# Performance work log

Measured on AMD Instinct MI355X. Metric: run time of the kernel, lower is better.

## Reference

```python
import jax, jax.numpy as jnp
import numpy as np

B, D, F, H = 256, 9, 8, 256   # batch of trees, tree depth, input features, hidden
N = 2 ** (D + 1) - 1          # total nodes per full binary tree (heap layout)


def _init(key, shape, fan_in):
    return jax.random.normal(key, shape, jnp.float32) * (1.0 / np.sqrt(fan_in))


def setup_inputs() -> dict:
    key = jax.random.key(0)
    ks = jax.random.split(key, 6)
    return {
        "data": jax.random.normal(ks[0], (B, N, F), jnp.float32),
        "Wu": _init(ks[1], (H, F), F),
        "bu": jnp.zeros((H,), jnp.float32),
        "Wr": _init(ks[2], (3 * H, 3 * H), 3 * H),
        "br": jnp.zeros((3 * H,), jnp.float32),
        "Wh": _init(ks[3], (H, 3 * H), 3 * H),
        "bh": jnp.zeros((H,), jnp.float32),
        "Wz": _init(ks[4], (4 * H, 4 * H), 4 * H),
        "bz": jnp.zeros((4 * H,), jnp.float32),
        "Wp": _init(ks[5], (1, H), H),
        "bp": jnp.zeros((1,), jnp.float32),
    }


def reference(data, Wu, bu, Wr, br, Wh, bh, Wz, bz, Wp, bp):
    # data: [B, N, F] node features in heap (level-order) layout;
    # children of the i-th node of level l are nodes 2i, 2i+1 of level l+1.
    b, n_nodes, _ = data.shape
    L = (n_nodes + 1) // 2          # number of leaves
    depth = L.bit_length() - 1
    h_dim = Wu.shape[0]

    # leaf embedding u for every node (leaf() is applied at every tree node)
    u = jnp.einsum('bnf,hf->bnh', data, Wu) + bu          # [B, N, H]
    h = u[:, L - 1:, :]                                    # leaf level states [B, L, H]

    for l in range(depth - 1, -1, -1):                     # bottom-up over levels
        n = 2 ** l
        parent = u[:, n - 1:2 * n - 1, :]                  # [B, n, H]
        h_l, h_r = h[:, 0::2, :], h[:, 1::2, :]            # [B, n, H] each
        hhu = jnp.concatenate([parent, h_l, h_r], axis=-1)  # [B, n, 3H]
        r = jax.nn.sigmoid(jnp.einsum('bnk,jk->bnj', hhu, Wr) + br)
        h_new = jax.nn.relu(jnp.einsum('bnk,hk->bnh', r * hhu, Wh) + bh)
        hhhu = jnp.concatenate([h_new, hhu], axis=-1)      # [B, n, 4H]
        zlin = jnp.einsum('bnk,jk->bnj', hhhu, Wz) + bz    # [B, n, 4H]
        z = jax.nn.softmax(zlin.reshape(b, n, 4, h_dim), axis=2)
        h = (z * hhhu.reshape(b, n, 4, h_dim)).sum(axis=2)  # gated combine -> [B, n, H]

    # h is [B, 1, H] at the root; logits head
    logits = jnp.einsum('bnh,oh->bno', h, Wp) + bp          # [B, 1, 1]
    return logits[:, 0, 0]                                  # [B]
```

## Files before the change

kernel.cpp:

```cpp
#include <hip/hip_runtime.h>
#include <math.h>

#define BB 256
#define NN 1023
#define FF 8
#define HH 256
#define DEPTH 9

enum { EPI_NONE = 0, EPI_SIGMUL = 1, EPI_RELU = 2, EPI_COMBINE = 3 };

typedef __bf16 bf16x8_t __attribute__((ext_vector_type(8)));
typedef float f32x4_t __attribute__((ext_vector_type(4)));

__device__ __forceinline__ void stage16(const void* g, void* l) {
    __builtin_amdgcn_global_load_lds(
        (const __attribute__((address_space(1))) void*)g,
        (__attribute__((address_space(3))) void*)l,
        16, 0, 0);
}

__device__ __forceinline__ int xcd_remap(int hw, int nwg) {
    const int xcd = hw & 7, k0 = hw >> 3;
    const int qq = nwg >> 3, rr = nwg & 7;
    return (xcd < rr ? xcd * (qq + 1) : rr * (qq + 1) + (xcd - rr) * qq) + k0;
}

template <int EPI>
__global__ __launch_bounds__(1024, 4) void gemm256w(
    const __bf16* __restrict__ A, int lda,
    const __bf16* __restrict__ W,
    const float* __restrict__ bias,
    const __bf16* __restrict__ aux, int ldaux,
    void* __restrict__ Cout, int ldc,
    int K)
{
    __shared__ __bf16 lds[2][2][256 * 64];
    const int tid = threadIdx.x;
    const int lane = tid & 63;
    const int w = tid >> 6;
    const int wr = w >> 2, wc = w & 3;

    const int nwg = gridDim.x * gridDim.y;
    const int hw = blockIdx.y * gridDim.x + blockIdx.x;
    const int wg = xcd_remap(hw, nwg);
    const int bm0 = (wg / gridDim.x) * 256;
    const int bn0 = (wg % gridDim.x) * 256;

    const int srow = tid >> 3;
    const int scolz = ((tid & 7) ^ (srow & 7)) * 8;

    f32x4_t acc[4][4];
#pragma unroll
    for (int i = 0; i < 4; ++i)
#pragma unroll
        for (int j = 0; j < 4; ++j) acc[i][j] = (f32x4_t){0.f, 0.f, 0.f, 0.f};

    const int rA = lane & 15;
    const int klane = (lane >> 4) * 8;
    const int rxor = (lane & 7) * 8;
    const int NT = K >> 6;

#define STAGE_T(t, buf)                                                        \
    do {                                                                       \
        const int kk_ = (t) << 6;                                              \
        stage16(A + (size_t)(bm0 + srow) * lda + kk_ + scolz,                  \
                &lds[buf][0][w * 512]);                                        \
        stage16(A + (size_t)(bm0 + 128 + srow) * lda + kk_ + scolz,            \
                &lds[buf][0][8192 + w * 512]);                                 \
        stage16(W + (size_t)(bn0 + srow) * K + kk_ + scolz,                    \
                &lds[buf][1][w * 512]);                                        \
        stage16(W + (size_t)(bn0 + 128 + srow) * K + kk_ + scolz,              \
                &lds[buf][1][8192 + w * 512]);                                 \
    } while (0)
#define LDA_F(As_, i, ks) \
    (*(const bf16x8_t*)&(As_)[(wr * 64 + (i) * 16 + rA) * 64 + (((ks) * 32 + klane) ^ rxor)])
#define LDB_F(Bs_, j, ks) \
    (*(const bf16x8_t*)&(Bs_)[(wc * 64 + (j) * 16 + rA) * 64 + (((ks) * 32 + klane) ^ rxor)])

    STAGE_T(0, 0);
    STAGE_T(1, 1);
    asm volatile("s_waitcnt vmcnt(4)" ::: "memory");
    __builtin_amdgcn_s_barrier();

    for (int t = 0; t < NT; ++t) {
        const int cur = t & 1;
        const __bf16* As = lds[cur][0];
        const __bf16* Bs = lds[cur][1];
        bf16x8_t af[4], bf[4];

#pragma unroll
        for (int j = 0; j < 4; ++j) bf[j] = LDB_F(Bs, j, 0);
#pragma unroll
        for (int i = 0; i < 4; ++i) af[i] = LDA_F(As, i, 0);
#pragma unroll
        for (int i = 0; i < 4; ++i)
#pragma unroll
            for (int j = 0; j < 4; ++j)
                acc[i][j] = __builtin_amdgcn_mfma_f32_16x16x32_bf16(
                    af[i], bf[j], acc[i][j], 0, 0, 0);
#pragma unroll
        for (int j = 0; j < 4; ++j) bf[j] = LDB_F(Bs, j, 1);
#pragma unroll
        for (int i = 0; i < 4; ++i) af[i] = LDA_F(As, i, 1);
#pragma unroll
        for (int i = 0; i < 2; ++i)
#pragma unroll
            for (int j = 0; j < 4; ++j)
                acc[i][j] = __builtin_amdgcn_mfma_f32_16x16x32_bf16(
                    af[i], bf[j], acc[i][j], 0, 0, 0);

        asm volatile("s_waitcnt lgkmcnt(0)" ::: "memory");
        __builtin_amdgcn_s_barrier();
        if (t + 2 < NT) STAGE_T(t + 2, cur);

        __builtin_amdgcn_s_setprio(1);
#pragma unroll
        for (int i = 2; i < 4; ++i)
#pragma unroll
            for (int j = 0; j < 4; ++j)
                acc[i][j] = __builtin_amdgcn_mfma_f32_16x16x32_bf16(
                    af[i], bf[j], acc[i][j], 0, 0, 0);
        __builtin_amdgcn_s_setprio(0);

        if (t + 1 < NT) {
            if (t + 2 < NT) {
                asm volatile("s_waitcnt vmcnt(4)" ::: "memory");
            } else {
                asm volatile("s_waitcnt vmcnt(0)" ::: "memory");
            }
            __builtin_amdgcn_s_barrier();
        }
    }
#undef STAGE_T
#undef LDA_F
#undef LDB_F

    const int hi = lane >> 4;
    const int r = lane & 15;

    if (EPI == EPI_COMBINE) {
        __bf16* pan = &lds[0][0][0];
        const int g0 = bn0 >> 2;
        float bz4[4];
#pragma unroll
        for (int g = 0; g < 4; ++g) bz4[g] = bias[bn0 + wc * 64 + g * 16 + r];
        const int G = g0 + wc * 16 + r;
#pragma unroll
        for (int i = 0; i < 4; ++i) {
#pragma unroll
            for (int reg = 0; reg < 4; ++reg) {
                const int lr = wr * 64 + i * 16 + hi * 4 + reg;
                const int gr = bm0 + lr;
                float z0 = acc[i][0][reg] + bz4[0];
                float z1 = acc[i][1][reg] + bz4[1];
                float z2 = acc[i][2][reg] + bz4[2];
                float z3 = acc[i][3][reg] + bz4[3];
                float mx = fmaxf(fmaxf(z0, z1), fmaxf(z2, z3));
                float e0 = __expf(z0 - mx), e1 = __expf(z1 - mx);
                float e2 = __expf(z2 - mx), e3 = __expf(z3 - mx);
                const __bf16* hrow = aux + (size_t)gr * ldaux + G;
                float hv = (e0 * (float)hrow[0] + e1 * (float)hrow[256] +
                            e2 * (float)hrow[512] + e3 * (float)hrow[768]) /
                           (e0 + e1 + e2 + e3);
                pan[lr * 72 + wc * 16 + r] = (__bf16)hv;
            }
        }
        __syncthreads();
#pragma unroll
        for (int it = 0; it < 2; ++it) {
            const int unit = it * 1024 + tid;
            const int row = unit >> 3;
            const int c8 = (unit & 7) * 8;
            bf16x8_t vv = *(const bf16x8_t*)&pan[row * 72 + c8];
            *(bf16x8_t*)((__bf16*)Cout + (size_t)(bm0 + row) * ldc + g0 + c8) = vv;
        }
    } else if (EPI == EPI_SIGMUL) {
        __bf16* pan = &lds[0][0][0];
        float bv[4];
#pragma unroll
        for (int j = 0; j < 4; ++j) bv[j] = bias[bn0 + wc * 64 + j * 16 + r];
#pragma unroll
        for (int j = 0; j < 4; ++j) {
            const int lc = wc * 64 + j * 16 + r;
            const int gc = bn0 + lc;
#pragma unroll
            for (int i = 0; i < 4; ++i) {
#pragma unroll
                for (int reg = 0; reg < 4; ++reg) {
                    const int lr = wr * 64 + i * 16 + hi * 4 + reg;
                    const int gr = bm0 + lr;
                    float v = acc[i][j][reg] + bv[j];
                    float s = 1.0f / (1.0f + __expf(-v));
                    v = s * (float)aux[(size_t)gr * ldaux + gc];
                    pan[lr * 256 + lc] = (__bf16)v;
                }
            }
        }
        __syncthreads();
#pragma unroll
        for (int it = 0; it < 8; ++it) {
            const int unit = it * 1024 + tid;
            const int row = unit >> 5;
            const int c8 = (unit & 31) * 8;
            bf16x8_t vv = *(const bf16x8_t*)&pan[row * 256 + c8];
            *(bf16x8_t*)((__bf16*)Cout + (size_t)(bm0 + row) * ldc + bn0 + c8) = vv;
        }
    } else {
#pragma unroll
        for (int j = 0; j < 4; ++j) {
            const int gc = bn0 + wc * 64 + j * 16 + r;
            const float bv = bias[gc];
#pragma unroll
            for (int i = 0; i < 4; ++i) {
#pragma unroll
                for (int reg = 0; reg < 4; ++reg) {
                    const int gr = bm0 + wr * 64 + i * 16 + hi * 4 + reg;
                    float v = acc[i][j][reg] + bv;
                    if (EPI == EPI_RELU) v = fmaxf(v, 0.0f);
                    if (EPI == EPI_RELU)
                        ((__bf16*)Cout)[(size_t)gr * ldc + gc] = (__bf16)v;
                    else
                        ((float*)Cout)[(size_t)gr * ldc + gc] = v;
                }
            }
        }
    }
}

template <int EPI>
__global__ __launch_bounds__(256) void gemm_mfma(
    const __bf16* __restrict__ A, int lda,
    const __bf16* __restrict__ W,
    const float* __restrict__ bias,
    const __bf16* __restrict__ aux, int ldaux,
    void* __restrict__ Cout, int ldc,
    int K)
{
    __shared__ __bf16 As[128 * 32];
    __shared__ __bf16 Bs[128 * 32];
    const int tid = threadIdx.x;
    const int lane = tid & 63;
    const int w = tid >> 6;
    const int wr = w >> 1, wc = w & 1;

    const int nwg = gridDim.x * gridDim.y;
    const int hw = blockIdx.y * gridDim.x + blockIdx.x;
    const int wg = xcd_remap(hw, nwg);
    const int bm0 = (wg / gridDim.x) * 128;
    const int bn0 = (wg % gridDim.x) * 128;

    const int srow = lane >> 2;
    const int scol = (lane & 3) * 8;

    f32x4_t acc[4][4];
#pragma unroll
    for (int i = 0; i < 4; ++i)
#pragma unroll
        for (int j = 0; j < 4; ++j) acc[i][j] = (f32x4_t){0.f, 0.f, 0.f, 0.f};

    const int rA = lane & 15;
    const int kslot = (lane >> 4) * 8;

    for (int kk = 0; kk < K; kk += 32) {
        stage16(A + (size_t)(bm0 + w * 16 + srow) * lda + kk + scol,
                &As[(w * 16) * 32]);
        stage16(A + (size_t)(bm0 + 64 + w * 16 + srow) * lda + kk + scol,
                &As[(64 + w * 16) * 32]);
        stage16(W + (size_t)(bn0 + w * 16 + srow) * K + kk + scol,
                &Bs[(w * 16) * 32]);
        stage16(W + (size_t)(bn0 + 64 + w * 16 + srow) * K + kk + scol,
                &Bs[(64 + w * 16) * 32]);
        __syncthreads();

        bf16x8_t af[4], bfr[4];
#pragma unroll
        for (int i = 0; i < 4; ++i)
            af[i] = *(const bf16x8_t*)&As[(wr * 64 + i * 16 + rA) * 32 + kslot];
#pragma unroll
        for (int j = 0; j < 4; ++j)
            bfr[j] = *(const bf16x8_t*)&Bs[(wc * 64 + j * 16 + rA) * 32 + kslot];
#pragma unroll
        for (int i = 0; i < 4; ++i)
#pragma unroll
            for (int j = 0; j < 4; ++j)
                acc[i][j] = __builtin_amdgcn_mfma_f32_16x16x32_bf16(
                    af[i], bfr[j], acc[i][j], 0, 0, 0);
        __syncthreads();
    }

    if (EPI == EPI_COMBINE) {
        const int r = lane & 15;
        const int G = ((bn0 + wc * 64) >> 2) + r;
        float bz4[4];
#pragma unroll
        for (int g = 0; g < 4; ++g) bz4[g] = bias[bn0 + wc * 64 + g * 16 + r];
#pragma unroll
        for (int i = 0; i < 4; ++i) {
#pragma unroll
            for (int reg = 0; reg < 4; ++reg) {
                const int gr = bm0 + wr * 64 + i * 16 + (lane >> 4) * 4 + reg;
                float z0 = acc[i][0][reg] + bz4[0];
                float z1 = acc[i][1][reg] + bz4[1];
                float z2 = acc[i][2][reg] + bz4[2];
                float z3 = acc[i][3][reg] + bz4[3];
                float mx = fmaxf(fmaxf(z0, z1), fmaxf(z2, z3));
                float e0 = __expf(z0 - mx), e1 = __expf(z1 - mx);
                float e2 = __expf(z2 - mx), e3 = __expf(z3 - mx);
                const __bf16* hrow = aux + (size_t)gr * ldaux + G;
                float hv = (e0 * (float)hrow[0] + e1 * (float)hrow[256] +
                            e2 * (float)hrow[512] + e3 * (float)hrow[768]) /
                           (e0 + e1 + e2 + e3);
                ((__bf16*)Cout)[(size_t)gr * ldc + G] = (__bf16)hv;
            }
        }
    } else {
#pragma unroll
        for (int j = 0; j < 4; ++j) {
            const int gc = bn0 + wc * 64 + j * 16 + (lane & 15);
            const float bv = bias[gc];
#pragma unroll
            for (int i = 0; i < 4; ++i) {
#pragma unroll
                for (int reg = 0; reg < 4; ++reg) {
                    const int gr = bm0 + wr * 64 + i * 16 + (lane >> 4) * 4 + reg;
                    float v = acc[i][j][reg] + bv;
                    if (EPI == EPI_SIGMUL) {
                        float s = 1.0f / (1.0f + __expf(-v));
                        v = s * (float)aux[(size_t)gr * ldaux + gc];
                        ((__bf16*)Cout)[(size_t)gr * ldc + gc] = (__bf16)v;
                    } else if (EPI == EPI_RELU) {
                        v = fmaxf(v, 0.0f);
                        ((__bf16*)Cout)[(size_t)gr * ldc + gc] = (__bf16)v;
                    } else {
                        ((float*)Cout)[(size_t)gr * ldc + gc] = v;
                    }
                }
            }
        }
    }
}

__global__ __launch_bounds__(256) void convert_weights(
    const float* __restrict__ Wr, const float* __restrict__ Wh,
    const float* __restrict__ Wz, const float* __restrict__ bz,
    __bf16* __restrict__ Wrb, __bf16* __restrict__ Whb,
    __bf16* __restrict__ Wzb, float* __restrict__ bzp)
{
    const int NR = 768 * 768, NH2 = 256 * 768, NZ = 1024 * 1024;
    const int idx0 = blockIdx.x * 256 + threadIdx.x;
    for (int i = idx0; i < NR + NH2 + NZ; i += gridDim.x * 256) {
        if (i < NR) Wrb[i] = (__bf16)Wr[i];
        else if (i < NR + NH2) Whb[i - NR] = (__bf16)Wh[i - NR];
        else {
            const int z = i - NR - NH2;
            const int p = z >> 10, k = z & 1023;
            const int o = ((p >> 4) & 3) * 256 + (p >> 6) * 16 + (p & 15);
            Wzb[z] = (__bf16)Wz[(size_t)o * 1024 + k];
        }
    }
    if (idx0 < 1024) {
        const int p = idx0;
        const int o = ((p >> 4) & 3) * 256 + (p >> 6) * 16 + (p & 15);
        bzp[p] = bz[o];
    }
}

__global__ __launch_bounds__(256) void build_hhu(
    const float* __restrict__ data, const float* __restrict__ Wu,
    const float* __restrict__ bu, const __bf16* __restrict__ hprev,
    __bf16* __restrict__ hhhu, int l, int r0)
{
    const int n = 1 << l;
    const int blk = xcd_remap(blockIdx.x, gridDim.x);
    const int row = blk * 8 + (threadIdx.x >> 5);
    const int c0 = (threadIdx.x & 31) * 8;
    const int i = r0 + row;
    const int b = i >> l;
    const int m = i & (n - 1);

    float wv[8][8];
#pragma unroll
    for (int cc = 0; cc < 8; ++cc) {
        float4 w0 = *(const float4*)&Wu[(c0 + cc) * 8];
        float4 w1 = *(const float4*)&Wu[(c0 + cc) * 8 + 4];
        wv[cc][0] = w0.x; wv[cc][1] = w0.y; wv[cc][2] = w0.z; wv[cc][3] = w0.w;
        wv[cc][4] = w1.x; wv[cc][5] = w1.y; wv[cc][6] = w1.z; wv[cc][7] = w1.w;
    }
    float buv[8];
#pragma unroll
    for (int cc = 0; cc < 8; ++cc) buv[cc] = bu[c0 + cc];

    __bf16* rowp = hhhu + (size_t)row * 1024;

    {
        const float* dp = data + ((size_t)b * NN + (n - 1) + m) * FF;
        float4 d0 = *(const float4*)dp, d1 = *(const float4*)(dp + 4);
        float dv[8] = {d0.x, d0.y, d0.z, d0.w, d1.x, d1.y, d1.z, d1.w};
        bf16x8_t o;
#pragma unroll
        for (int cc = 0; cc < 8; ++cc) {
            float acc = buv[cc];
#pragma unroll
            for (int f = 0; f < 8; ++f) acc += dv[f] * wv[cc][f];
            o[cc] = (__bf16)acc;
        }
        *(bf16x8_t*)&rowp[256 + c0] = o;
    }

    if (l == 8) {
        const float* dl = data + ((size_t)b * NN + 511 + 2 * m) * FF;
#pragma unroll
        for (int side = 0; side < 2; ++side) {
            const float* dp = dl + side * FF;
            float4 d0 = *(const float4*)dp, d1 = *(const float4*)(dp + 4);
            float dv[8] = {d0.x, d0.y, d0.z, d0.w, d1.x, d1.y, d1.z, d1.w};
            bf16x8_t o;
#pragma unroll
            for (int cc = 0; cc < 8; ++cc) {
                float acc = buv[cc];
#pragma unroll
                for (int f = 0; f < 8; ++f) acc += dv[f] * wv[cc][f];
                o[cc] = (__bf16)acc;
            }
            *(bf16x8_t*)&rowp[512 + side * 256 + c0] = o;
        }
    } else {
        *(bf16x8_t*)&rowp[512 + c0] =
            *(const bf16x8_t*)&hprev[((size_t)b * (2 * n) + 2 * m) * HH + c0];
        *(bf16x8_t*)&rowp[768 + c0] =
            *(const bf16x8_t*)&hprev[((size_t)b * (2 * n) + 2 * m + 1) * HH + c0];
    }
}

__global__ __launch_bounds__(256) void final_kernel(
    const __bf16* __restrict__ hfin, const float* __restrict__ Wp,
    const float* __restrict__ bp, float* __restrict__ out)
{
    const int b = blockIdx.x;
    const int t = threadIdx.x;
    __shared__ float red[256];
    red[t] = (float)hfin[(size_t)b * HH + t] * Wp[t];
    __syncthreads();
    for (int s = 128; s > 0; s >>= 1) {
        if (t < s) red[t] += red[t + s];
        __syncthreads();
    }
    if (t == 0) out[b] = red[0] + bp[0];
}

extern "C" void kernel_launch(void* const* d_in, const int* in_sizes, int n_in,
                              void* d_out, int out_size, void* d_ws, size_t ws_size,
                              hipStream_t stream)
{
    const float* data = (const float*)d_in[0];
    const float* Wu = (const float*)d_in[1];
    const float* bu = (const float*)d_in[2];
    const float* Wr = (const float*)d_in[3];
    const float* br = (const float*)d_in[4];
    const float* Wh = (const float*)d_in[5];
    const float* bh = (const float*)d_in[6];
    const float* Wz = (const float*)d_in[7];
    const float* bz = (const float*)d_in[8];
    const float* Wp = (const float*)d_in[9];
    const float* bp = (const float*)d_in[10];
    float* out = (float*)d_out;

    const size_t CAP = 16384;
    char* w = (char*)d_ws;
    __bf16* hA = (__bf16*)w;   w += (size_t)65536 * HH * 2;
    __bf16* hB = (__bf16*)w;   w += (size_t)32768 * HH * 2;
    __bf16* hhhu = (__bf16*)w; w += CAP * 1024 * 2;
    __bf16* rh = (__bf16*)w;   w += CAP * 768 * 2;
    __bf16* Wrb = (__bf16*)w;  w += (size_t)768 * 768 * 2;
    __bf16* Whb = (__bf16*)w;  w += (size_t)256 * 768 * 2;
    __bf16* Wzb = (__bf16*)w;  w += (size_t)1024 * 1024 * 2;
    float* bzp = (float*)w;    w += 1024 * 4;

    convert_weights<<<2048, 256, 0, stream>>>(Wr, Wh, Wz, bz, Wrb, Whb, Wzb, bzp);

    for (int l = DEPTH - 1; l >= 0; --l) {
        const size_t M = (size_t)BB << l;
        __bf16* dst = ((DEPTH - 1 - l) & 1) ? hB : hA;
        const __bf16* src = ((DEPTH - 1 - l) & 1) ? hA : hB;
        for (size_t r0 = 0; r0 < M; r0 += CAP) {
            const int R = (int)((M - r0 < CAP) ? (M - r0) : CAP);
            build_hhu<<<R / 8, 256, 0, stream>>>(data, Wu, bu, src, hhhu, l, (int)r0);
            if (R >= 16384) {
                gemm256w<EPI_SIGMUL><<<dim3(3, R / 256), 1024, 0, stream>>>(
                    hhhu + 256, 1024, Wrb, br, hhhu + 256, 1024, rh, 768, 768);
            } else {
                gemm_mfma<EPI_SIGMUL><<<dim3(6, R / 128), 256, 0, stream>>>(
                    hhhu + 256, 1024, Wrb, br, hhhu + 256, 1024, rh, 768, 768);
            }
            gemm_mfma<EPI_RELU><<<dim3(2, R / 128), 256, 0, stream>>>(
                rh, 768, Whb, bh, nullptr, 0, hhhu, 1024, 768);
            if (R >= 16384) {
                gemm256w<EPI_COMBINE><<<dim3(4, R / 256), 1024, 0, stream>>>(
                    hhhu, 1024, Wzb, bzp, hhhu, 1024,
                    dst + (size_t)r0 * HH, HH, 1024);
            } else {
                gemm_mfma<EPI_COMBINE><<<dim3(8, R / 128), 256, 0, stream>>>(
                    hhhu, 1024, Wzb, bzp, hhhu, 1024,
                    dst + (size_t)r0 * HH, HH, 1024);
            }
        }
    }
    final_kernel<<<BB, 256, 0, stream>>>(hA, Wp, bp, out);
}
```

Before: 1.186 ms.

## Write combine output directly into parent level's hhhu buffer, drop child copy

The combine GEMM epilogue now scatters each node's new hidden state straight into the child slots (columns 512/768) of the next level's full-width hhhu buffer, indexed by row parity. This removes the separate h buffers and the copy of child states that build_hhu did, so non-leaf levels only compute the u embedding. The cost is much larger workspace (full 1024-wide buffers for two levels) and scattered half-row writes in the epilogue. The gemm256w combine path always writes to the parent layout, which holds because it only runs for l>0.

```diff
diff --git a/kernel.cpp b/kernel.cpp
--- a/kernel.cpp
+++ b/kernel.cpp
@@ -32,6 +32,7 @@
     const float* __restrict__ bias,
     const __bf16* __restrict__ aux, int ldaux,
     void* __restrict__ Cout, int ldc,
+    int r0c,
     int K)
 {
     __shared__ __bf16 lds[2][2][256 * 64];
@@ -166,13 +167,16 @@
             }
         }
         __syncthreads();
+        const int cbase = r0c + bm0;
 #pragma unroll
         for (int it = 0; it < 2; ++it) {
             const int unit = it * 1024 + tid;
             const int row = unit >> 3;
             const int c8 = (unit & 7) * 8;
+            const int crow = cbase + row;
             bf16x8_t vv = *(const bf16x8_t*)&pan[row * 72 + c8];
-            *(bf16x8_t*)((__bf16*)Cout + (size_t)(bm0 + row) * ldc + g0 + c8) = vv;
+            *(bf16x8_t*)((__bf16*)Cout + (size_t)(crow >> 1) * 1024 + 512 +
+                         (crow & 1) * 256 + g0 + c8) = vv;
         }
     } else if (EPI == EPI_SIGMUL) {
         __bf16* pan = &lds[0][0][0];
@@ -217,10 +221,7 @@
                     const int gr = bm0 + wr * 64 + i * 16 + hi * 4 + reg;
                     float v = acc[i][j][reg] + bv;
                     if (EPI == EPI_RELU) v = fmaxf(v, 0.0f);
-                    if (EPI == EPI_RELU)
-                        ((__bf16*)Cout)[(size_t)gr * ldc + gc] = (__bf16)v;
-                    else
-                        ((float*)Cout)[(size_t)gr * ldc + gc] = v;
+                    ((__bf16*)Cout)[(size_t)gr * ldc + gc] = (__bf16)v;
                 }
             }
         }
@@ -234,6 +235,7 @@
     const float* __restrict__ bias,
     const __bf16* __restrict__ aux, int ldaux,
     void* __restrict__ Cout, int ldc,
+    int r0c, int topar,
     int K)
 {
     __shared__ __bf16 As[128 * 32];
@@ -310,7 +312,13 @@
                 float hv = (e0 * (float)hrow[0] + e1 * (float)hrow[256] +
                             e2 * (float)hrow[512] + e3 * (float)hrow[768]) /
                            (e0 + e1 + e2 + e3);
-                ((__bf16*)Cout)[(size_t)gr * ldc + G] = (__bf16)hv;
+                if (topar) {
+                    const int crow = r0c + gr;
+                    ((__bf16*)Cout)[(size_t)(crow >> 1) * 1024 + 512 +
+                                    (crow & 1) * 256 + G] = (__bf16)hv;
+                } else {
+                    ((__bf16*)Cout)[(size_t)gr * ldc + G] = (__bf16)hv;
+                }
             }
         }
     } else {
@@ -365,10 +373,65 @@
     }
 }
 
-__global__ __launch_bounds__(256) void build_hhu(
+__global__ __launch_bounds__(256) void build_leaf(
     const float* __restrict__ data, const float* __restrict__ Wu,
-    const float* __restrict__ bu, const __bf16* __restrict__ hprev,
-    __bf16* __restrict__ hhhu, int l, int r0)
+    const float* __restrict__ bu, __bf16* __restrict__ slice, int r0)
+{
+    const int blk = xcd_remap(blockIdx.x, gridDim.x);
+    const int row = blk * 8 + (threadIdx.x >> 5);
+    const int c0 = (threadIdx.x & 31) * 8;
+    const int i = r0 + row;
+    const int b = i >> 8;
+    const int m = i & 255;
+
+    float wv[8][8];
+#pragma unroll
+    for (int cc = 0; cc < 8; ++cc) {
+        float4 w0 = *(const float4*)&Wu[(c0 + cc) * 8];
+        float4 w1 = *(const float4*)&Wu[(c0 + cc) * 8 + 4];
+        wv[cc][0] = w0.x; wv[cc][1] = w0.y; wv[cc][2] = w0.z; wv[cc][3] = w0.w;
+        wv[cc][4] = w1.x; wv[cc][5] = w1.y; wv[cc][6] = w1.z; wv[cc][7] = w1.w;
+    }
+    float buv[8];
+#pragma unroll
+    for (int cc = 0; cc < 8; ++cc) buv[cc] = bu[c0 + cc];
+
+    __bf16* rowp = slice + (size_t)row * 1024;
+    {
+        const float* dp = data + ((size_t)b * NN + 255 + m) * FF;
+        float4 d0 = *(const float4*)dp, d1 = *(const float4*)(dp + 4);
+        float dv[8] = {d0.x, d0.y, d0.z, d0.w, d1.x, d1.y, d1.z, d1.w};
+        bf16x8_t o;
+#pragma unroll
+        for (int cc = 0; cc < 8; ++cc) {
+            float acc = buv[cc];
+#pragma unroll
+            for (int f = 0; f < 8; ++f) acc += dv[f] * wv[cc][f];
+            o[cc] = (__bf16)acc;
+        }
+        *(bf16x8_t*)&rowp[256 + c0] = o;
+    }
+    const float* dl = data + ((size_t)b * NN + 511 + 2 * m) * FF;
+#pragma unroll
+    for (int side = 0; side < 2; ++side) {
+        const float* dp = dl + side * FF;
+        float4 d0 = *(const float4*)dp, d1 = *(const float4*)(dp + 4);
+        float dv[8] = {d0.x, d0.y, d0.z, d0.w, d1.x, d1.y, d1.z, d1.w};
+        bf16x8_t o;
+#pragma unroll
+        for (int cc = 0; cc < 8; ++cc) {
+            float acc = buv[cc];
+#pragma unroll
+            for (int f = 0; f < 8; ++f) acc += dv[f] * wv[cc][f];
+            o[cc] = (__bf16)acc;
+        }
+        *(bf16x8_t*)&rowp[512 + side * 256 + c0] = o;
+    }
+}
+
+__global__ __launch_bounds__(256) void build_u(
+    const float* __restrict__ data, const float* __restrict__ Wu,
+    const float* __restrict__ bu, __bf16* __restrict__ slice, int l, int r0)
 {
     const int n = 1 << l;
     const int blk = xcd_remap(blockIdx.x, gridDim.x);
@@ -386,50 +449,18 @@
         wv[cc][0] = w0.x; wv[cc][1] = w0.y; wv[cc][2] = w0.z; wv[cc][3] = w0.w;
         wv[cc][4] = w1.x; wv[cc][5] = w1.y; wv[cc][6] = w1.z; wv[cc][7] = w1.w;
     }
-    float buv[8];
-#pragma unroll
-    for (int cc = 0; cc < 8; ++cc) buv[cc] = bu[c0 + cc];
-
-    __bf16* rowp = hhhu + (size_t)row * 1024;
-
-    {
-        const float* dp = data + ((size_t)b * NN + (n - 1) + m) * FF;
-        float4 d0 = *(const float4*)dp, d1 = *(const float4*)(dp + 4);
-        float dv[8] = {d0.x, d0.y, d0.z, d0.w, d1.x, d1.y, d1.z, d1.w};
-        bf16x8_t o;
-#pragma unroll
-        for (int cc = 0; cc < 8; ++cc) {
-            float acc = buv[cc];
-#pragma unroll
-            for (int f = 0; f < 8; ++f) acc += dv[f] * wv[cc][f];
-            o[cc] = (__bf16)acc;
-        }
-        *(bf16x8_t*)&rowp[256 + c0] = o;
-    }
-
-    if (l == 8) {
-        const float* dl = data + ((size_t)b * NN + 511 + 2 * m) * FF;
-#pragma unroll
-        for (int side = 0; side < 2; ++side) {
-            const float* dp = dl + side * FF;
-            float4 d0 = *(const float4*)dp, d1 = *(const float4*)(dp + 4);
-            float dv[8] = {d0.x, d0.y, d0.z, d0.w, d1.x, d1.y, d1.z, d1.w};
-            bf16x8_t o;
-#pragma unroll
-            for (int cc = 0; cc < 8; ++cc) {
-                float acc = buv[cc];
-#pragma unroll
-                for (int f = 0; f < 8; ++f) acc += dv[f] * wv[cc][f];
-                o[cc] = (__bf16)acc;
-            }
-            *(bf16x8_t*)&rowp[512 + side * 256 + c0] = o;
-        }
-    } else {
-        *(bf16x8_t*)&rowp[512 + c0] =
-            *(const bf16x8_t*)&hprev[((size_t)b * (2 * n) + 2 * m) * HH + c0];
-        *(bf16x8_t*)&rowp[768 + c0] =
-            *(const bf16x8_t*)&hprev[((size_t)b * (2 * n) + 2 * m + 1) * HH + c0];
-    }
+    const float* dp = data + ((size_t)b * NN + (n - 1) + m) * FF;
+    float4 d0 = *(const float4*)dp, d1 = *(const float4*)(dp + 4);
+    float dv[8] = {d0.x, d0.y, d0.z, d0.w, d1.x, d1.y, d1.z, d1.w};
+    bf16x8_t o;
+#pragma unroll
+    for (int cc = 0; cc < 8; ++cc) {
+        float acc = bu[c0 + cc];
+#pragma unroll
+        for (int f = 0; f < 8; ++f) acc += dv[f] * wv[cc][f];
+        o[cc] = (__bf16)acc;
+    }
+    *(bf16x8_t*)&slice[(size_t)row * 1024 + 256 + c0] = o;
 }
 
 __global__ __launch_bounds__(256) void final_kernel(
@@ -467,43 +498,46 @@
 
     const size_t CAP = 16384;
     char* w = (char*)d_ws;
-    __bf16* hA = (__bf16*)w;   w += (size_t)65536 * HH * 2;
-    __bf16* hB = (__bf16*)w;   w += (size_t)32768 * HH * 2;
-    __bf16* hhhu = (__bf16*)w; w += CAP * 1024 * 2;
-    __bf16* rh = (__bf16*)w;   w += CAP * 768 * 2;
-    __bf16* Wrb = (__bf16*)w;  w += (size_t)768 * 768 * 2;
-    __bf16* Whb = (__bf16*)w;  w += (size_t)256 * 768 * 2;
-    __bf16* Wzb = (__bf16*)w;  w += (size_t)1024 * 1024 * 2;
-    float* bzp = (float*)w;    w += 1024 * 4;
+    __bf16* hhhuA = (__bf16*)w; w += (size_t)65536 * 1024 * 2;
+    __bf16* hhhuB = (__bf16*)w; w += (size_t)32768 * 1024 * 2;
+    __bf16* rh = (__bf16*)w;    w += CAP * 768 * 2;
+    __bf16* hRoot = (__bf16*)w; w += (size_t)256 * 256 * 2;
+    __bf16* Wrb = (__bf16*)w;   w += (size_t)768 * 768 * 2;
+    __bf16* Whb = (__bf16*)w;   w += (size_t)256 * 768 * 2;
+    __bf16* Wzb = (__bf16*)w;   w += (size_t)1024 * 1024 * 2;
+    float* bzp = (float*)w;     w += 1024 * 4;
 
     convert_weights<<<2048, 256, 0, stream>>>(Wr, Wh, Wz, bz, Wrb, Whb, Wzb, bzp);
 
     for (int l = DEPTH - 1; l >= 0; --l) {
         const size_t M = (size_t)BB << l;
-        __bf16* dst = ((DEPTH - 1 - l) & 1) ? hB : hA;
-        const __bf16* src = ((DEPTH - 1 - l) & 1) ? hA : hB;
+        __bf16* cur = (l & 1) ? hhhuB : hhhuA;
+        __bf16* par = (l == 0) ? hRoot : ((l & 1) ? hhhuA : hhhuB);
+        const int topar = (l > 0);
         for (size_t r0 = 0; r0 < M; r0 += CAP) {
             const int R = (int)((M - r0 < CAP) ? (M - r0) : CAP);
-            build_hhu<<<R / 8, 256, 0, stream>>>(data, Wu, bu, src, hhhu, l, (int)r0);
+            __bf16* slice = cur + (size_t)r0 * 1024;
+            if (l == 8)
+                build_leaf<<<R / 8, 256, 0, stream>>>(data, Wu, bu, slice, (int)r0);
+            else
+                build_u<<<R / 8, 256, 0, stream>>>(data, Wu, bu, slice, l, (int)r0);
             if (R >= 16384) {
                 gemm256w<EPI_SIGMUL><<<dim3(3, R / 256), 1024, 0, stream>>>(
-                    hhhu + 256, 1024, Wrb, br, hhhu + 256, 1024, rh, 768, 768);
+                    slice + 256, 1024, Wrb, br, slice + 256, 1024, rh, 768, 0, 768);
             } else {
                 gemm_mfma<EPI_SIGMUL><<<dim3(6, R / 128), 256, 0, stream>>>(
-                    hhhu + 256, 1024, Wrb, br, hhhu + 256, 1024, rh, 768, 768);
+                    slice + 256, 1024, Wrb, br, slice + 256, 1024, rh, 768, 0, 0, 768);
             }
             gemm_mfma<EPI_RELU><<<dim3(2, R / 128), 256, 0, stream>>>(
-                rh, 768, Whb, bh, nullptr, 0, hhhu, 1024, 768);
+                rh, 768, Whb, bh, nullptr, 0, slice, 1024, 0, 0, 768);
             if (R >= 16384) {
                 gemm256w<EPI_COMBINE><<<dim3(4, R / 256), 1024, 0, stream>>>(
-                    hhhu, 1024, Wzb, bzp, hhhu, 1024,
-                    dst + (size_t)r0 * HH, HH, 1024);
+                    slice, 1024, Wzb, bzp, slice, 1024, par, HH, (int)r0, 1024);
             } else {
                 gemm_mfma<EPI_COMBINE><<<dim3(8, R / 128), 256, 0, stream>>>(
-                    hhhu, 1024, Wzb, bzp, hhhu, 1024,
-                    dst + (size_t)r0 * HH, HH, 1024);
-            }
-        }
-    }
-    final_kernel<<<BB, 256, 0, stream>>>(hA, Wp, bp, out);
-}
+                    slice, 1024, Wzb, bzp, slice, 1024, par, HH, (int)r0, topar, 1024);
+            }
+        }
+    }
+    final_kernel<<<BB, 256, 0, stream>>>(hRoot, Wp, bp, out);
+}
```

New measurement: 1.176 ms (median of 2 runs). No clear change (-0.8%).
